# Optimization experiments

Measured on AMD Instinct MI355X. Metric: run time of the kernel, lower is better.

## Reference

```python
import jax, jax.numpy as jnp
import numpy as np

EP = 1e-4
EPMAX = 30.0
RTOL, ATOL = 1e-5, 1e-8  # torch.allclose defaults


def _safe(n):
    return jnp.where(n == 0, 1.0, n)


def _rigid_from_3(x):
    # x: (L, 3, 3) -> rot (L,3,3) rows e1,e2,e3 ; origin (L,3)
    x1, x2, x3 = x[:, 0], x[:, 1], x[:, 2]
    v1 = x3 - x2
    v2 = x1 - x2
    e1 = v1 / (jnp.linalg.norm(v1, axis=-1, keepdims=True) + 1e-3)
    u2 = v2 - e1 * jnp.einsum('ld,ld->l', e1, v2)[:, None]
    e2 = u2 / (jnp.linalg.norm(u2, axis=-1, keepdims=True) + 1e-8)
    e3 = jnp.cross(e1, e2)
    return jnp.stack([e1, e2, e3], axis=1), x2


def _merge_frames(rot, trans, ii, jj):
    # Vectorized merge_coordinate_systems over all selected pairs (ii, jj).
    O_A, O_B = trans[ii], trans[jj]          # (P,3)
    RA, RB = rot[ii], rot[jj]                # (P,3,3)
    close = jnp.all(jnp.abs(O_A - O_B) <= ATOL + RTOL * jnp.abs(O_B), axis=-1)
    d = O_B - O_A
    nd = jnp.linalg.norm(d, axis=-1)
    X_new = d / _safe(nd)[:, None]
    Z_add = RA[:, 2] + RB[:, 2]
    Z_sub = RA[:, 2] - RB[:, 2]
    na = jnp.linalg.norm(Z_add, axis=-1)
    ns = jnp.linalg.norm(Z_sub, axis=-1)
    Z_new = jnp.where((na > ns)[:, None], Z_add / _safe(na)[:, None], Z_sub / _safe(ns)[:, None])
    Y_new = jnp.cross(Z_new, X_new)
    nan_bad = jnp.any(jnp.isnan(Y_new), axis=-1)
    flip = jnp.einsum('pd,pd->p', jnp.cross(X_new, Y_new), Z_new) < 0
    Y_new = jnp.where(flip[:, None], -Y_new, Y_new)
    R_new = jnp.stack([X_new, Y_new, Z_new], axis=1)  # (P,3,3)
    O_new = 0.5 * (O_A + O_B)
    bad = close | (nd == 0) | (na == 0) | (ns == 0) | nan_bad
    R_out = jnp.where(bad[:, None, None], RA, R_new)
    O_out = jnp.where(bad[:, None], O_A, O_new)
    return jnp.concatenate([rot, R_out], axis=0), jnp.concatenate([trans, O_out], axis=0)


def _frame_transform(points, rot, tran):
    # points: (N,3); rot: (F,3,3); tran: (F,3) -> (N,F,3)
    diff = points[:, None, :] - tran[None, :, :]
    return jnp.einsum('nfd,fed->nfe', diff, rot)


def setup_inputs():
    key = jax.random.key(0)
    k0, k1, k2, k3 = jax.random.split(key, 4)
    L = 1024
    coor = 5.0 * jax.random.normal(k0, (L, 3, 3), jnp.float32)
    # valid orthonormal frames from random points
    rot, _ = _rigid_from_3(5.0 * jax.random.normal(k1, (L, 3, 3), jnp.float32))
    trans = 5.0 * jax.random.normal(k2, (L, 3), jnp.float32)
    target = 5.0 * jax.random.normal(k3, (L, 3, 3), jnp.float32)
    idx = np.arange(L)
    band = idx[None, :] - idx[:, None]
    matrix = ((band > 0) & (band <= 8)).astype(np.int32)  # ~8k contact pairs
    return {"coor": coor, "rot": rot, "trans": trans, "target": target,
            "matrix": jnp.asarray(matrix)}


def reference(coor, rot, trans, target, matrix):
    m = np.asarray(matrix)
    ii_np, jj_np = np.nonzero(np.triu(m, 1) == 1)
    ii, jj = jnp.asarray(ii_np), jnp.asarray(jj_np)
    p_rot, p_tran = _merge_frames(rot, trans, ii, jj)
    pred_x2 = _frame_transform(coor.reshape(-1, 3), p_rot, p_tran)   # (N,F,3)
    t_rot0, t_tran0 = _rigid_from_3(target)
    t_rot, t_tran = _merge_frames(t_rot0, t_tran0, ii, jj)
    tx = _frame_transform(target.reshape(-1, 3), t_rot, t_tran)     # (N,F,3)
    errmap = jnp.sqrt(jnp.sum((pred_x2 - tx) ** 2 + EP, axis=-1))
    return jnp.mean(jnp.minimum(errmap, EPMAX))
```

## Files before the change

kernel.cpp:

```cpp
#include <hip/hip_runtime.h>

#define EPV    0.0001f
#define EPMAXV 30.0f
#define RTOLV  1e-5f
#define ATOLV  1e-8f
#define NPART  1024
#define CHUNK  112


__device__ inline void write_rec(float* __restrict__ rec,
                                 const float Rp[9], const float Op[3],
                                 const float Rt[9], const float Ot[3]) {
    float P[9], N[9];
#pragma unroll
    for (int k = 0; k < 9; k++) { P[k] = Rp[k]; N[k] = -Rt[k]; }
    float kx = -(P[0] * Op[0] + P[1] * Op[1] + P[2] * Op[2]
               + N[0] * Ot[0] + N[1] * Ot[1] + N[2] * Ot[2]);
    float ky = -(P[3] * Op[0] + P[4] * Op[1] + P[5] * Op[2]
               + N[3] * Ot[0] + N[4] * Ot[1] + N[5] * Ot[2]);
    float kz = -(P[6] * Op[0] + P[7] * Op[1] + P[8] * Op[2]
               + N[6] * Ot[0] + N[7] * Ot[1] + N[8] * Ot[2]);
    float4* r4 = (float4*)rec;
    r4[0] = make_float4(P[0], P[1], P[2], P[3]);
    r4[1] = make_float4(P[4], P[5], P[6], P[7]);
    r4[2] = make_float4(P[8], N[0], N[1], N[2]);
    r4[3] = make_float4(N[3], N[4], N[5], N[6]);
    r4[4] = make_float4(N[7], N[8], kx, ky);
    r4[5] = make_float4(kz, 0.f, 0.f, 0.f);
}

__global__ void k_prep(const int* __restrict__ m, int L, unsigned int* __restrict__ rowcnt,
                       const float* __restrict__ rot, const float* __restrict__ trans,
                       const float* __restrict__ target, int nrb,
                       float* __restrict__ pF, float* __restrict__ tF,
                       float* __restrict__ rec) {
    if ((int)blockIdx.x < nrb) {
        int i = blockIdx.x * 4 + (threadIdx.x >> 6);
        if (i >= L) return;
        int lane = threadIdx.x & 63;
        const int* row = m + (size_t)i * L;
        unsigned int c = 0;
        for (int j0 = 0; j0 < L; j0 += 64) {
            int j = j0 + lane;
            bool v = (j < L) && (j > i) && (row[j] == 1);
            unsigned long long b = __ballot(v);
            c += (unsigned int)__popcll(b);
        }
        if (lane == 0) rowcnt[i] = c;
        return;
    }
    int l = ((int)blockIdx.x - nrb) * 256 + threadIdx.x;
    if (l >= L) return;
    float Rp[9], Op[3];
#pragma unroll
    for (int k = 0; k < 9; k++) Rp[k] = rot[l * 9 + k];
#pragma unroll
    for (int k = 0; k < 3; k++) Op[k] = trans[l * 3 + k];
    float* pf = pF + l * 12;
#pragma unroll
    for (int k = 0; k < 9; k++) pf[k] = Rp[k];
#pragma unroll
    for (int k = 0; k < 3; k++) pf[9 + k] = Op[k];
    const float* tg = target + l * 9;
    float x1x = tg[0], x1y = tg[1], x1z = tg[2];
    float x2x = tg[3], x2y = tg[4], x2z = tg[5];
    float x3x = tg[6], x3y = tg[7], x3z = tg[8];
    float v1x = x3x - x2x, v1y = x3y - x2y, v1z = x3z - x2z;
    float v2x = x1x - x2x, v2y = x1y - x2y, v2z = x1z - x2z;
    float n1 = sqrtf(v1x * v1x + v1y * v1y + v1z * v1z) + 0.001f;
    float e1x = v1x / n1, e1y = v1y / n1, e1z = v1z / n1;
    float c = e1x * v2x + e1y * v2y + e1z * v2z;
    float u2x = v2x - c * e1x, u2y = v2y - c * e1y, u2z = v2z - c * e1z;
    float n2 = sqrtf(u2x * u2x + u2y * u2y + u2z * u2z) + 1e-8f;
    float e2x = u2x / n2, e2y = u2y / n2, e2z = u2z / n2;
    float Rt[9], Ot[3];
    Rt[0] = e1x; Rt[1] = e1y; Rt[2] = e1z;
    Rt[3] = e2x; Rt[4] = e2y; Rt[5] = e2z;
    Rt[6] = e1y * e2z - e1z * e2y;
    Rt[7] = e1z * e2x - e1x * e2z;
    Rt[8] = e1x * e2y - e1y * e2x;
    Ot[0] = x2x; Ot[1] = x2y; Ot[2] = x2z;
    float* tf = tF + l * 12;
#pragma unroll
    for (int k = 0; k < 9; k++) tf[k] = Rt[k];
#pragma unroll
    for (int k = 0; k < 3; k++) tf[9 + k] = Ot[k];
    write_rec(rec + (size_t)l * 24, Rp, Op, Rt, Ot);
}

__device__ inline void merge_frames(const float* __restrict__ A, const float* __restrict__ B,
                                    float R[9], float O[3]) {
    const float* RA = A; const float* OA = A + 9;
    const float* RB = B; const float* OB = B + 9;
    bool close = (fabsf(OA[0] - OB[0]) <= ATOLV + RTOLV * fabsf(OB[0])) &&
                 (fabsf(OA[1] - OB[1]) <= ATOLV + RTOLV * fabsf(OB[1])) &&
                 (fabsf(OA[2] - OB[2]) <= ATOLV + RTOLV * fabsf(OB[2]));
    float d0 = OB[0] - OA[0], d1 = OB[1] - OA[1], d2 = OB[2] - OA[2];
    float nd = sqrtf(d0 * d0 + d1 * d1 + d2 * d2);
    float nds = (nd == 0.f) ? 1.f : nd;
    float X0 = d0 / nds, X1 = d1 / nds, X2 = d2 / nds;
    float Za0 = RA[6] + RB[6], Za1 = RA[7] + RB[7], Za2 = RA[8] + RB[8];
    float Zs0 = RA[6] - RB[6], Zs1 = RA[7] - RB[7], Zs2 = RA[8] - RB[8];
    float na = sqrtf(Za0 * Za0 + Za1 * Za1 + Za2 * Za2);
    float ns = sqrtf(Zs0 * Zs0 + Zs1 * Zs1 + Zs2 * Zs2);
    float nas = (na == 0.f) ? 1.f : na;
    float nss = (ns == 0.f) ? 1.f : ns;
    float Z0, Z1, Z2;
    if (na > ns) { Z0 = Za0 / nas; Z1 = Za1 / nas; Z2 = Za2 / nas; }
    else         { Z0 = Zs0 / nss; Z1 = Zs1 / nss; Z2 = Zs2 / nss; }
    float Y0 = Z1 * X2 - Z2 * X1;
    float Y1 = Z2 * X0 - Z0 * X2;
    float Y2 = Z0 * X1 - Z1 * X0;
    bool nanbad = (Y0 != Y0) || (Y1 != Y1) || (Y2 != Y2);
    float C0 = X1 * Y2 - X2 * Y1;
    float C1 = X2 * Y0 - X0 * Y2;
    float C2 = X0 * Y1 - X1 * Y0;
    float dotv = C0 * Z0 + C1 * Z1 + C2 * Z2;
    if (dotv < 0.f) { Y0 = -Y0; Y1 = -Y1; Y2 = -Y2; }
    bool bad = close || (nd == 0.f) || (na == 0.f) || (ns == 0.f) || nanbad;
    if (bad) {
#pragma unroll
        for (int k = 0; k < 9; k++) R[k] = RA[k];
#pragma unroll
        for (int k = 0; k < 3; k++) O[k] = OA[k];
    } else {
        R[0] = X0; R[1] = X1; R[2] = X2;
        R[3] = Y0; R[4] = Y1; R[5] = Y2;
        R[6] = Z0; R[7] = Z1; R[8] = Z2;
        O[0] = 0.5f * (OA[0] + OB[0]);
        O[1] = 0.5f * (OA[1] + OB[1]);
        O[2] = 0.5f * (OA[2] + OB[2]);
    }
}

__global__ void k_fillmerge(const int* __restrict__ m, int L,
                            const unsigned int* __restrict__ rowcnt,
                            unsigned int* __restrict__ count, int cap,
                            const float* __restrict__ pF, const float* __restrict__ tF,
                            float* __restrict__ rec) {
    int i = blockIdx.x * 4 + (threadIdx.x >> 6);
    int lane = threadIdx.x & 63;

    if (blockIdx.x == 0 && (threadIdx.x >> 6) == 0) {
        unsigned int t = 0;
        for (int r = lane; r < L; r += 64) t += rowcnt[r];
#pragma unroll
        for (int off = 1; off < 64; off <<= 1) t += __shfl_xor(t, off, 64);
        if (lane == 0) *count = t;
    }
    if (i >= L) return;

    unsigned int p = 0;
    for (int r = lane; r < i; r += 64) p += rowcnt[r];
#pragma unroll
    for (int off = 1; off < 64; off <<= 1) p += __shfl_xor(p, off, 64);
    unsigned int base = p;

    const int* row = m + (size_t)i * L;
    unsigned long long lt = (lane == 0) ? 0ull : ((1ull << lane) - 1ull);
    for (int j0 = 0; j0 < L; j0 += 64) {
        int j = j0 + lane;
        bool v = (j < L) && (j > i) && (row[j] == 1);
        unsigned long long b = __ballot(v);
        if (v) {
            unsigned int pos = base + (unsigned int)__popcll(b & lt);
            if (pos < (unsigned int)cap) {
                float Rp[9], Op[3], Rt[9], Ot[3];
                merge_frames(pF + i * 12, pF + j * 12, Rp, Op);
                merge_frames(tF + i * 12, tF + j * 12, Rt, Ot);
                write_rec(rec + (size_t)(L + pos) * 24, Rp, Op, Rt, Ot);
            }
        }
        base += (unsigned int)__popcll(b);
    }
}

__global__ __launch_bounds__(256, 4)
void k_main(const float* __restrict__ coor, const float* __restrict__ target,
            const float* __restrict__ rec, const unsigned int* __restrict__ count,
            int cap, int L, int Npts, double* __restrict__ partials) {
    __shared__ float4 sC[CHUNK];
    __shared__ float4 sT[CHUNK];
    __shared__ float sRed[4];
    unsigned int cnt = *count;
    if (cnt > (unsigned int)cap) cnt = (unsigned int)cap;
    int F = L + (int)cnt;
    int nfb = (F + 255) >> 8;
    int nyc = (Npts + CHUNK - 1) / CHUNK;
    int total = nfb * nyc;
    float a0 = 0.f, a1 = 0.f;

    for (int chunk = blockIdx.x; chunk < total; chunk += gridDim.x) {
        int fb = chunk % nfb;
        int yc = chunk / nfb;
        int n0 = yc * CHUNK;
        int npts = Npts - n0; if (npts > CHUNK) npts = CHUNK;
        __syncthreads();
        for (int idx = threadIdx.x; idx < npts; idx += 256) {
            int g = (n0 + idx) * 3;
            sC[idx] = make_float4(coor[g], coor[g + 1], coor[g + 2], 0.f);
            sT[idx] = make_float4(target[g], target[g + 1], target[g + 2], 0.f);
        }
        __syncthreads();
        int f = fb * 256 + threadIdx.x;
        if (f >= F) continue;

        const float4* fr = (const float4*)(rec + (size_t)f * 24);
        float4 r0 = fr[0], r1 = fr[1], r2 = fr[2], r3 = fr[3], r4 = fr[4], r5 = fr[5];
        float P00 = r0.x, P01 = r0.y, P02 = r0.z;
        float P10 = r0.w, P11 = r1.x, P12 = r1.y;
        float P20 = r1.z, P21 = r1.w, P22 = r2.x;
        float N00 = r2.y, N01 = r2.z, N02 = r2.w;
        float N10 = r3.x, N11 = r3.y, N12 = r3.z;
        float N20 = r3.w, N21 = r4.x, N22 = r4.y;
        float kx  = r4.z, ky  = r4.w, kz  = r5.x;

#pragma unroll 4
        for (int n = 0; n < npts; n++) {
            float4 c = sC[n];
            float4 t = sT[n];
            float ux = kx + P00 * c.x + P01 * c.y + P02 * c.z
                          + N00 * t.x + N01 * t.y + N02 * t.z;
            float uy = ky + P10 * c.x + P11 * c.y + P12 * c.z
                          + N10 * t.x + N11 * t.y + N12 * t.z;
            float uz = kz + P20 * c.x + P21 * c.y + P22 * c.z
                          + N20 * t.x + N21 * t.y + N22 * t.z;
            float s = ux * ux + uy * uy + uz * uz + 3.0f * EPV;
            float r = fminf(__builtin_amdgcn_sqrtf(s), EPMAXV);
            if (n & 1) a1 += r; else a0 += r;
        }
    }

    float a = a0 + a1;
#pragma unroll
    for (int off = 32; off > 0; off >>= 1) a += __shfl_down(a, off, 64);
    int lane = threadIdx.x & 63, wv = threadIdx.x >> 6;
    if (lane == 0) sRed[wv] = a;
    __syncthreads();
    if (threadIdx.x == 0)
        partials[blockIdx.x] = (double)(sRed[0] + sRed[1] + sRed[2] + sRed[3]);
}

__global__ void k_final(const double* __restrict__ partials, int npart,
                        const unsigned int* __restrict__ count, int cap,
                        int L, int Npts, float* __restrict__ out) {
    __shared__ double sR[4];
    double d = 0.0;
    for (int i = threadIdx.x; i < npart; i += 256) d += partials[i];
#pragma unroll
    for (int off = 32; off > 0; off >>= 1) d += __shfl_down(d, off, 64);
    int lane = threadIdx.x & 63, wv = threadIdx.x >> 6;
    if (lane == 0) sR[wv] = d;
    __syncthreads();
    if (threadIdx.x == 0) {
        double tot = sR[0] + sR[1] + sR[2] + sR[3];
        unsigned int cnt = *count;
        if (cnt > (unsigned int)cap) cnt = (unsigned int)cap;
        double F = (double)(L + (int)cnt);
        out[0] = (float)(tot / ((double)Npts * F));
    }
}

extern "C" void kernel_launch(void* const* d_in, const int* in_sizes, int n_in,
                              void* d_out, int out_size, void* d_ws, size_t ws_size,
                              hipStream_t stream) {
    const float* coor   = (const float*)d_in[0];
    const float* rot    = (const float*)d_in[1];
    const float* trans  = (const float*)d_in[2];
    const float* target = (const float*)d_in[3];
    const int*   matrix = (const int*)d_in[4];
    int L    = in_sizes[2] / 3;
    int Npts = 3 * L;

    char* ws = (char*)d_ws;
    size_t off = 16;
    unsigned int* count  = (unsigned int*)ws;
    unsigned int* rowcnt = (unsigned int*)(ws + off); off += 4 * (size_t)L;
    off = (off + 15) & ~(size_t)15;
    double* partials = (double*)(ws + off); off += 8 * (size_t)NPART;
    off = (off + 15) & ~(size_t)15;
    float* pF = (float*)(ws + off); off += 48 * (size_t)L;
    float* tF = (float*)(ws + off); off += 48 * (size_t)L;
    off = (off + 15) & ~(size_t)15;
    long cap_ws = ((long)ws_size - (long)off - 96L * (long)L) / 96;
    long capl = cap_ws < 32768 ? cap_ws : 32768;
    if (capl < 0) capl = 0;
    int cap = (int)capl;
    float* rec = (float*)(ws + off);

    int nrb   = (L + 3) / 4;
    int nbase = (L + 255) / 256;
    k_prep<<<nrb + nbase, 256, 0, stream>>>(matrix, L, rowcnt, rot, trans, target,
                                            nrb, pF, tF, rec);
    k_fillmerge<<<nrb, 256, 0, stream>>>(matrix, L, rowcnt, count, cap, pF, tF, rec);
    k_main<<<NPART, 256, 0, stream>>>(coor, target, rec, count, cap, L, Npts, partials);
    k_final<<<1, 256, 0, stream>>>(partials, NPART, count, cap, L, Npts, (float*)d_out);
}
```

Baseline: 107.2 us.

## Fuse four kernels into one cooperative kernel with grid-wide syncs

Merges the prep, fill/merge, main, and final-reduction kernels into a single cooperative launch, using grid.sync() between phases instead of separate kernel launches. It also vectorizes the row-count scan with int4 loads and a shuffle reduction in place of ballots. The aim is to remove three launch gaps and their dependency bubbles. In exchange it pays for three grid-wide barriers and needs all 1024 blocks to be co-resident; at 4 blocks per CU that is at the limit of the device, and the cooperative launch fails otherwise.

```diff
diff --git a/kernel.cpp b/kernel.cpp
--- a/kernel.cpp
+++ b/kernel.cpp
@@ -1,4 +1,7 @@
 #include <hip/hip_runtime.h>
+#include <hip/hip_cooperative_groups.h>
+
+namespace cg = cooperative_groups;
 
 #define EPV    0.0001f
 #define EPMAXV 30.0f
@@ -27,65 +30,6 @@
     r4[3] = make_float4(N[3], N[4], N[5], N[6]);
     r4[4] = make_float4(N[7], N[8], kx, ky);
     r4[5] = make_float4(kz, 0.f, 0.f, 0.f);
-}
-
-__global__ void k_prep(const int* __restrict__ m, int L, unsigned int* __restrict__ rowcnt,
-                       const float* __restrict__ rot, const float* __restrict__ trans,
-                       const float* __restrict__ target, int nrb,
-                       float* __restrict__ pF, float* __restrict__ tF,
-                       float* __restrict__ rec) {
-    if ((int)blockIdx.x < nrb) {
-        int i = blockIdx.x * 4 + (threadIdx.x >> 6);
-        if (i >= L) return;
-        int lane = threadIdx.x & 63;
-        const int* row = m + (size_t)i * L;
-        unsigned int c = 0;
-        for (int j0 = 0; j0 < L; j0 += 64) {
-            int j = j0 + lane;
-            bool v = (j < L) && (j > i) && (row[j] == 1);
-            unsigned long long b = __ballot(v);
-            c += (unsigned int)__popcll(b);
-        }
-        if (lane == 0) rowcnt[i] = c;
-        return;
-    }
-    int l = ((int)blockIdx.x - nrb) * 256 + threadIdx.x;
-    if (l >= L) return;
-    float Rp[9], Op[3];
-#pragma unroll
-    for (int k = 0; k < 9; k++) Rp[k] = rot[l * 9 + k];
-#pragma unroll
-    for (int k = 0; k < 3; k++) Op[k] = trans[l * 3 + k];
-    float* pf = pF + l * 12;
-#pragma unroll
-    for (int k = 0; k < 9; k++) pf[k] = Rp[k];
-#pragma unroll
-    for (int k = 0; k < 3; k++) pf[9 + k] = Op[k];
-    const float* tg = target + l * 9;
-    float x1x = tg[0], x1y = tg[1], x1z = tg[2];
-    float x2x = tg[3], x2y = tg[4], x2z = tg[5];
-    float x3x = tg[6], x3y = tg[7], x3z = tg[8];
-    float v1x = x3x - x2x, v1y = x3y - x2y, v1z = x3z - x2z;
-    float v2x = x1x - x2x, v2y = x1y - x2y, v2z = x1z - x2z;
-    float n1 = sqrtf(v1x * v1x + v1y * v1y + v1z * v1z) + 0.001f;
-    float e1x = v1x / n1, e1y = v1y / n1, e1z = v1z / n1;
-    float c = e1x * v2x + e1y * v2y + e1z * v2z;
-    float u2x = v2x - c * e1x, u2y = v2y - c * e1y, u2z = v2z - c * e1z;
-    float n2 = sqrtf(u2x * u2x + u2y * u2y + u2z * u2z) + 1e-8f;
-    float e2x = u2x / n2, e2y = u2y / n2, e2z = u2z / n2;
-    float Rt[9], Ot[3];
-    Rt[0] = e1x; Rt[1] = e1y; Rt[2] = e1z;
-    Rt[3] = e2x; Rt[4] = e2y; Rt[5] = e2z;
-    Rt[6] = e1y * e2z - e1z * e2y;
-    Rt[7] = e1z * e2x - e1x * e2z;
-    Rt[8] = e1x * e2y - e1y * e2x;
-    Ot[0] = x2x; Ot[1] = x2y; Ot[2] = x2z;
-    float* tf = tF + l * 12;
-#pragma unroll
-    for (int k = 0; k < 9; k++) tf[k] = Rt[k];
-#pragma unroll
-    for (int k = 0; k < 3; k++) tf[9 + k] = Ot[k];
-    write_rec(rec + (size_t)l * 24, Rp, Op, Rt, Ot);
 }
 
 __device__ inline void merge_frames(const float* __restrict__ A, const float* __restrict__ B,
@@ -133,55 +77,116 @@
     }
 }
 
-__global__ void k_fillmerge(const int* __restrict__ m, int L,
-                            const unsigned int* __restrict__ rowcnt,
-                            unsigned int* __restrict__ count, int cap,
-                            const float* __restrict__ pF, const float* __restrict__ tF,
-                            float* __restrict__ rec) {
-    int i = blockIdx.x * 4 + (threadIdx.x >> 6);
-    int lane = threadIdx.x & 63;
-
-    if (blockIdx.x == 0 && (threadIdx.x >> 6) == 0) {
+__global__ __launch_bounds__(256, 4)
+void k_all(const int* __restrict__ m, int L,
+           const float* __restrict__ rot, const float* __restrict__ trans,
+           const float* __restrict__ target, const float* __restrict__ coor,
+           unsigned int* __restrict__ rowcnt, unsigned int* __restrict__ count,
+           float* __restrict__ pF, float* __restrict__ tF, float* __restrict__ rec,
+           int cap, int Npts, double* __restrict__ partials, float* __restrict__ out) {
+    cg::grid_group grid = cg::this_grid();
+    __shared__ float4 sC[CHUNK];
+    __shared__ float4 sT[CHUNK];
+    __shared__ float  sRed[4];
+    __shared__ double sRd[4];
+
+    const int nrb   = (L + 3) / 4;
+    const int nbase = (L + 255) / 256;
+    const int lane  = threadIdx.x & 63;
+    const int wv    = threadIdx.x >> 6;
+
+    if ((int)blockIdx.x < nrb) {
+        int i = blockIdx.x * 4 + wv;
+        if (i < L) {
+            const int4* row4 = (const int4*)(m + (size_t)i * L);
+            unsigned int c = 0;
+            for (int b = lane; b * 4 < L; b += 64) {
+                int4 v = row4[b];
+                int j = b * 4;
+                c += (unsigned)((j + 0 > i) & (v.x == 1)) + (unsigned)((j + 1 > i) & (v.y == 1))
+                   + (unsigned)((j + 2 > i) & (v.z == 1)) + (unsigned)((j + 3 > i) & (v.w == 1));
+            }
+#pragma unroll
+            for (int off = 1; off < 64; off <<= 1) c += __shfl_xor(c, off, 64);
+            if (lane == 0) rowcnt[i] = c;
+        }
+    } else if ((int)blockIdx.x < nrb + nbase) {
+        int l = ((int)blockIdx.x - nrb) * 256 + threadIdx.x;
+        if (l < L) {
+            float Rp[9], Op[3];
+#pragma unroll
+            for (int k = 0; k < 9; k++) Rp[k] = rot[l * 9 + k];
+#pragma unroll
+            for (int k = 0; k < 3; k++) Op[k] = trans[l * 3 + k];
+            float* pf = pF + l * 12;
+#pragma unroll
+            for (int k = 0; k < 9; k++) pf[k] = Rp[k];
+#pragma unroll
+            for (int k = 0; k < 3; k++) pf[9 + k] = Op[k];
+            const float* tg = target + l * 9;
+            float x1x = tg[0], x1y = tg[1], x1z = tg[2];
+            float x2x = tg[3], x2y = tg[4], x2z = tg[5];
+            float x3x = tg[6], x3y = tg[7], x3z = tg[8];
+            float v1x = x3x - x2x, v1y = x3y - x2y, v1z = x3z - x2z;
+            float v2x = x1x - x2x, v2y = x1y - x2y, v2z = x1z - x2z;
+            float n1 = sqrtf(v1x * v1x + v1y * v1y + v1z * v1z) + 0.001f;
+            float e1x = v1x / n1, e1y = v1y / n1, e1z = v1z / n1;
+            float c = e1x * v2x + e1y * v2y + e1z * v2z;
+            float u2x = v2x - c * e1x, u2y = v2y - c * e1y, u2z = v2z - c * e1z;
+            float n2 = sqrtf(u2x * u2x + u2y * u2y + u2z * u2z) + 1e-8f;
+            float e2x = u2x / n2, e2y = u2y / n2, e2z = u2z / n2;
+            float Rt[9], Ot[3];
+            Rt[0] = e1x; Rt[1] = e1y; Rt[2] = e1z;
+            Rt[3] = e2x; Rt[4] = e2y; Rt[5] = e2z;
+            Rt[6] = e1y * e2z - e1z * e2y;
+            Rt[7] = e1z * e2x - e1x * e2z;
+            Rt[8] = e1x * e2y - e1y * e2x;
+            Ot[0] = x2x; Ot[1] = x2y; Ot[2] = x2z;
+            float* tf = tF + l * 12;
+#pragma unroll
+            for (int k = 0; k < 9; k++) tf[k] = Rt[k];
+#pragma unroll
+            for (int k = 0; k < 3; k++) tf[9 + k] = Ot[k];
+            write_rec(rec + (size_t)l * 24, Rp, Op, Rt, Ot);
+        }
+    }
+    grid.sync();
+
+    if ((int)blockIdx.x < nrb) {
+        int i = blockIdx.x * 4 + wv;
+        if (i < L) {
+            unsigned int p = 0;
+            for (int r = lane; r < i; r += 64) p += rowcnt[r];
+#pragma unroll
+            for (int off = 1; off < 64; off <<= 1) p += __shfl_xor(p, off, 64);
+            unsigned int base = p;
+            const int* row = m + (size_t)i * L;
+            unsigned long long lt = (lane == 0) ? 0ull : ((1ull << lane) - 1ull);
+            for (int j0 = 0; j0 < L; j0 += 64) {
+                int j = j0 + lane;
+                bool v = (j < L) && (j > i) && (row[j] == 1);
+                unsigned long long b = __ballot(v);
+                if (v) {
+                    unsigned int pos = base + (unsigned int)__popcll(b & lt);
+                    if (pos < (unsigned int)cap) {
+                        float Rp[9], Op[3], Rt[9], Ot[3];
+                        merge_frames(pF + i * 12, pF + j * 12, Rp, Op);
+                        merge_frames(tF + i * 12, tF + j * 12, Rt, Ot);
+                        write_rec(rec + (size_t)(L + pos) * 24, Rp, Op, Rt, Ot);
+                    }
+                }
+                base += (unsigned int)__popcll(b);
+            }
+        }
+    } else if ((int)blockIdx.x == nrb && wv == 0) {
         unsigned int t = 0;
         for (int r = lane; r < L; r += 64) t += rowcnt[r];
 #pragma unroll
         for (int off = 1; off < 64; off <<= 1) t += __shfl_xor(t, off, 64);
         if (lane == 0) *count = t;
     }
-    if (i >= L) return;
-
-    unsigned int p = 0;
-    for (int r = lane; r < i; r += 64) p += rowcnt[r];
-#pragma unroll
-    for (int off = 1; off < 64; off <<= 1) p += __shfl_xor(p, off, 64);
-    unsigned int base = p;
-
-    const int* row = m + (size_t)i * L;
-    unsigned long long lt = (lane == 0) ? 0ull : ((1ull << lane) - 1ull);
-    for (int j0 = 0; j0 < L; j0 += 64) {
-        int j = j0 + lane;
-        bool v = (j < L) && (j > i) && (row[j] == 1);
-        unsigned long long b = __ballot(v);
-        if (v) {
-            unsigned int pos = base + (unsigned int)__popcll(b & lt);
-            if (pos < (unsigned int)cap) {
-                float Rp[9], Op[3], Rt[9], Ot[3];
-                merge_frames(pF + i * 12, pF + j * 12, Rp, Op);
-                merge_frames(tF + i * 12, tF + j * 12, Rt, Ot);
-                write_rec(rec + (size_t)(L + pos) * 24, Rp, Op, Rt, Ot);
-            }
-        }
-        base += (unsigned int)__popcll(b);
-    }
-}
-
-__global__ __launch_bounds__(256, 4)
-void k_main(const float* __restrict__ coor, const float* __restrict__ target,
-            const float* __restrict__ rec, const unsigned int* __restrict__ count,
-            int cap, int L, int Npts, double* __restrict__ partials) {
-    __shared__ float4 sC[CHUNK];
-    __shared__ float4 sT[CHUNK];
-    __shared__ float sRed[4];
+    grid.sync();
+
     unsigned int cnt = *count;
     if (cnt > (unsigned int)cap) cnt = (unsigned int)cap;
     int F = L + (int)cnt;
@@ -234,30 +239,24 @@
     float a = a0 + a1;
 #pragma unroll
     for (int off = 32; off > 0; off >>= 1) a += __shfl_down(a, off, 64);
-    int lane = threadIdx.x & 63, wv = threadIdx.x >> 6;
+    __syncthreads();
     if (lane == 0) sRed[wv] = a;
     __syncthreads();
     if (threadIdx.x == 0)
         partials[blockIdx.x] = (double)(sRed[0] + sRed[1] + sRed[2] + sRed[3]);
-}
-
-__global__ void k_final(const double* __restrict__ partials, int npart,
-                        const unsigned int* __restrict__ count, int cap,
-                        int L, int Npts, float* __restrict__ out) {
-    __shared__ double sR[4];
-    double d = 0.0;
-    for (int i = threadIdx.x; i < npart; i += 256) d += partials[i];
-#pragma unroll
-    for (int off = 32; off > 0; off >>= 1) d += __shfl_down(d, off, 64);
-    int lane = threadIdx.x & 63, wv = threadIdx.x >> 6;
-    if (lane == 0) sR[wv] = d;
-    __syncthreads();
-    if (threadIdx.x == 0) {
-        double tot = sR[0] + sR[1] + sR[2] + sR[3];
-        unsigned int cnt = *count;
-        if (cnt > (unsigned int)cap) cnt = (unsigned int)cap;
-        double F = (double)(L + (int)cnt);
-        out[0] = (float)(tot / ((double)Npts * F));
+    grid.sync();
+
+    if (blockIdx.x == 0) {
+        double d = 0.0;
+        for (int i = threadIdx.x; i < (int)gridDim.x; i += 256) d += partials[i];
+#pragma unroll
+        for (int off = 32; off > 0; off >>= 1) d += __shfl_down(d, off, 64);
+        if (lane == 0) sRd[wv] = d;
+        __syncthreads();
+        if (threadIdx.x == 0) {
+            double tot = sRd[0] + sRd[1] + sRd[2] + sRd[3];
+            out[0] = (float)(tot / ((double)Npts * (double)F));
+        }
     }
 }
 
@@ -288,11 +287,10 @@
     int cap = (int)capl;
     float* rec = (float*)(ws + off);
 
-    int nrb   = (L + 3) / 4;
-    int nbase = (L + 255) / 256;
-    k_prep<<<nrb + nbase, 256, 0, stream>>>(matrix, L, rowcnt, rot, trans, target,
-                                            nrb, pF, tF, rec);
-    k_fillmerge<<<nrb, 256, 0, stream>>>(matrix, L, rowcnt, count, cap, pF, tF, rec);
-    k_main<<<NPART, 256, 0, stream>>>(coor, target, rec, count, cap, L, Npts, partials);
-    k_final<<<1, 256, 0, stream>>>(partials, NPART, count, cap, L, Npts, (float*)d_out);
-}
+    void* args[] = {
+        (void*)&matrix, (void*)&L, (void*)&rot, (void*)&trans, (void*)&target,
+        (void*)&coor, (void*)&rowcnt, (void*)&count, (void*)&pF, (void*)&tF,
+        (void*)&rec, (void*)&cap, (void*)&Npts, (void*)&partials, (void*)&d_out
+    };
+    hipLaunchCooperativeKernel((void*)k_all, dim3(NPART), dim3(256), args, 0, stream);
+}
```

Measured after the change: 371.3 us. 3.46x slower.
